# Kernel tuning notes

Hardware: AMD Instinct MI355X
Metric: run time of the kernel (lower is better)

## Reference

```python
import jax, jax.numpy as jnp
import numpy as np

B, NJ, NT, F = 1024, 24, 6, 64
H = 128        # edge/classification MLP hidden width
NODE_OUT = 64  # node MLP output width
REG_OUT = 4


def _mlp2(x, W1, b1, W2, b2):
    h = jax.nn.relu(x @ W1 + b1)
    return jax.nn.relu(h @ W2 + b2)


def _edges(recv, send):
    # broadcast-concat edge formation: (B, Nr, Ns, Fr+Fs)
    Bb, Nr, Fr = recv.shape
    Ns, Fs = send.shape[1], send.shape[2]
    r = jnp.broadcast_to(recv[:, :, None, :], (Bb, Nr, Ns, Fr))
    s = jnp.broadcast_to(send[:, None, :, :], (Bb, Nr, Ns, Fs))
    return jnp.concatenate([r, s], axis=-1)


def _masked_mean(e, mask_send):
    # average-pool edges over sender axis, honoring sender mask
    if mask_send is None:
        return jnp.mean(e, axis=2)
    m = mask_send[:, None, :, :]  # (B,1,Ns,1)
    return jnp.sum(e * m, axis=2) / jnp.maximum(jnp.sum(m, axis=2), 1.0)


def setup_inputs() -> dict:
    key = jax.random.key(0)
    ks = jax.random.split(key, 32)
    g = lambda k, sh, sc: jax.random.normal(k, sh, dtype=jnp.float32) * sc
    inp = {
        "jets": g(ks[0], (B, NJ, F), 1.0),
        "mask": (jax.random.uniform(ks[1], (B, NJ, 1)) < 0.85).astype(jnp.float32),
        "nodes_top": g(ks[2], (B, NT, F), 1.0),
    }
    # edge networks (input = concat of two node feature vectors = 2F)
    for i, name in enumerate(["jj", "jt", "tj"]):
        inp[f"W_{name}1"] = g(ks[3 + 2 * i], (2 * F, H), (2.0 / (2 * F)) ** 0.5)
        inp[f"b_{name}1"] = jnp.zeros((H,), jnp.float32)
        inp[f"W_{name}2"] = g(ks[4 + 2 * i], (H, H), (2.0 / H) ** 0.5)
        inp[f"b_{name}2"] = jnp.zeros((H,), jnp.float32)
    # node networks
    inp["Wnj1"] = g(ks[10], (F + 2 * H, H), (2.0 / (F + 2 * H)) ** 0.5)
    inp["bnj1"] = jnp.zeros((H,), jnp.float32)
    inp["Wnj2"] = g(ks[11], (H, NODE_OUT), (2.0 / H) ** 0.5)
    inp["bnj2"] = jnp.zeros((NODE_OUT,), jnp.float32)
    inp["Wnt1"] = g(ks[12], (F + H, H), (2.0 / (F + H)) ** 0.5)
    inp["bnt1"] = jnp.zeros((H,), jnp.float32)
    inp["Wnt2"] = g(ks[13], (H, NODE_OUT), (2.0 / H) ** 0.5)
    inp["bnt2"] = jnp.zeros((NODE_OUT,), jnp.float32)
    # edge classification network (input = concat of two updated nodes = 2*NODE_OUT)
    inp["Wc1"] = g(ks[14], (2 * NODE_OUT, H), (2.0 / (2 * NODE_OUT)) ** 0.5)
    inp["bc1"] = jnp.zeros((H,), jnp.float32)
    inp["Wc2"] = g(ks[15], (H, H), (2.0 / H) ** 0.5)
    inp["bc2"] = jnp.zeros((H,), jnp.float32)
    inp["Wc3"] = g(ks[16], (H, 1), (2.0 / H) ** 0.5)
    inp["bc3"] = jnp.zeros((1,), jnp.float32)
    inp["Wr1"] = g(ks[17], (NT, NODE_OUT, H), (2.0 / NODE_OUT) ** 0.5)
    inp["br1"] = jnp.zeros((NT, H), jnp.float32)
    inp["Wr2"] = g(ks[18], (NT, H, H), (2.0 / H) ** 0.5)
    inp["br2"] = jnp.zeros((NT, H), jnp.float32)
    inp["Wr3"] = g(ks[19], (NT, H, REG_OUT), (2.0 / H) ** 0.5)
    inp["br3"] = jnp.zeros((NT, REG_OUT), jnp.float32)
    return inp


def reference(jets, mask, nodes_top,
              W_jj1, b_jj1, W_jj2, b_jj2,
              W_jt1, b_jt1, W_jt2, b_jt2,
              W_tj1, b_tj1, W_tj2, b_tj2,
              Wnj1, bnj1, Wnj2, bnj2,
              Wnt1, bnt1, Wnt2, bnt2,
              Wc1, bc1, Wc2, bc2, Wc3, bc3,
              Wr1, br1, Wr2, br2, Wr3, br3):
    # --- TopoGraphLayer ---
    # jet-jet edges (fully connected), masked avg pool over sender jets
    e_jj = _mlp2(_edges(jets, jets), W_jj1, b_jj1, W_jj2, b_jj2)   # (B,NJ,NJ,H)
    pooled_jj = _masked_mean(e_jj, mask)                           # (B,NJ,H)
    # jet-top edges (all top nodes exist -> plain mean pool)
    e_jt = _mlp2(_edges(jets, nodes_top), W_jt1, b_jt1, W_jt2, b_jt2)  # (B,NJ,NT,H)
    pooled_jt = _masked_mean(e_jt, None)                           # (B,NJ,H)
    upd_jets = _mlp2(jnp.concatenate([jets, pooled_jj, pooled_jt], -1),
                     Wnj1, bnj1, Wnj2, bnj2) * mask                # pass_with_mask
    # top-jet edges, masked avg pool over sender jets
    e_tj = _mlp2(_edges(nodes_top, jets), W_tj1, b_tj1, W_tj2, b_tj2)  # (B,NT,NJ,H)
    pooled_tj = _masked_mean(e_tj, mask)                           # (B,NT,H)
    upd_tops = _mlp2(jnp.concatenate([nodes_top, pooled_tj], -1),
                     Wnt1, bnt1, Wnt2, bnt2)                       # (B,NT,NODE_OUT)
    # --- EdgeClassification (top <- jet edges on updated nodes) ---
    e_cls = _mlp2(_edges(upd_tops, upd_jets), Wc1, bc1, Wc2, bc2)  # (B,NT,NJ,H)
    edge_scores = jax.nn.sigmoid(e_cls @ Wc3 + bc3) * mask[:, None, :, :]  # (B,NT,NJ,1)
    # --- ParticlePredictionMLPs (one MLP per top node) ---
    h = jax.nn.relu(jnp.einsum('bpf,pfh->bph', upd_tops, Wr1) + br1)
    h = jax.nn.relu(jnp.einsum('bpf,pfh->bph', h, Wr2) + br2)
    regression = jnp.einsum('bpf,pfh->bph', h, Wr3) + br3          # (B,NT,REG_OUT)
    return upd_jets, upd_tops, edge_scores, regression
```

## Files before the change

### kernel.cpp

```cpp
#include <hip/hip_runtime.h>
#include <hip/hip_bf16.h>


#define DEVI __device__ __forceinline__

typedef __attribute__((ext_vector_type(4))) float  floatx4;
typedef __attribute__((ext_vector_type(8))) __bf16 bf16x8;
typedef __attribute__((ext_vector_type(4))) __bf16 bf16x4;

DEVI float4 f4z() { return make_float4(0.f, 0.f, 0.f, 0.f); }
DEVI float4 f4fma(float a, const float4 b, float4 c) {
    c.x = fmaf(a, b.x, c.x); c.y = fmaf(a, b.y, c.y);
    c.z = fmaf(a, b.z, c.z); c.w = fmaf(a, b.w, c.w);
    return c;
}
DEVI float4 f4add(float4 a, const float4 b) {
    a.x += b.x; a.y += b.y; a.z += b.z; a.w += b.w; return a;
}
DEVI float4 f4relu(float4 a) {
    a.x = fmaxf(a.x, 0.f); a.y = fmaxf(a.y, 0.f);
    a.z = fmaxf(a.z, 0.f); a.w = fmaxf(a.w, 0.f);
    return a;
}
DEVI floatx4 mfma_bf16(bf16x8 a, bf16x8 b, floatx4 c) {
    return __builtin_amdgcn_mfma_f32_16x16x32_bf16(a, b, c, 0, 0, 0);
}

struct PrepJob { const float* src; __bf16* dh; __bf16* dl; int K; int N; };
struct PrepJobs { PrepJob j[4]; };

__global__ __launch_bounds__(256) void prep_kernel(PrepJobs jobs) {
    const PrepJob jb = jobs.j[blockIdx.y];
    const int n = jb.K * jb.N;
    for (int i = blockIdx.x * 256 + threadIdx.x; i < n; i += gridDim.x * 256) {
        const int c = i / jb.K, k = i - c * jb.K;
        const float w = jb.src[(size_t)k * jb.N + c];
        const __bf16 h = (__bf16)w;
        jb.dh[i] = h;
        jb.dl[i] = (__bf16)(w - (float)h);
    }
}

struct PreCfg { const float* X; const float* W; const float* bias; float* out; int nrows; };
struct PreCfg6 { PreCfg c[6]; };

__global__ __launch_bounds__(256) void pre_gemm_kernel(PreCfg6 cfgs) {
    const PreCfg cfg = cfgs.c[blockIdx.y];
    if ((int)blockIdx.x * 32 >= cfg.nrows) return;
    __shared__ float Xs[32][64];
    __shared__ float Ws[64][128];
    const int tid = threadIdx.x;
    {
        const float4* s = (const float4*)(cfg.X + (size_t)blockIdx.x * 2048);
        float4* d = (float4*)&Xs[0][0];
        d[tid] = s[tid]; d[tid + 256] = s[tid + 256];
    }
    {
        const float4* s = (const float4*)cfg.W;
        float4* d = (float4*)&Ws[0][0];
        #pragma unroll
        for (int u = 0; u < 8; ++u) d[tid + u * 256] = s[tid + u * 256];
    }
    __syncthreads();
    const int cg = tid & 31, rg = tid >> 5;
    const int c0 = cg * 4, r0 = rg * 4;
    float4 acc[4] = {f4z(), f4z(), f4z(), f4z()};
    #pragma unroll 4
    for (int k = 0; k < 64; k += 4) {
        const float4 w0 = *(const float4*)&Ws[k + 0][c0];
        const float4 w1 = *(const float4*)&Ws[k + 1][c0];
        const float4 w2 = *(const float4*)&Ws[k + 2][c0];
        const float4 w3 = *(const float4*)&Ws[k + 3][c0];
        #pragma unroll
        for (int i = 0; i < 4; ++i) {
            const float4 x = *(const float4*)&Xs[r0 + i][k];
            acc[i] = f4fma(x.x, w0, acc[i]);
            acc[i] = f4fma(x.y, w1, acc[i]);
            acc[i] = f4fma(x.z, w2, acc[i]);
            acc[i] = f4fma(x.w, w3, acc[i]);
        }
    }
    const float4 bv = cfg.bias ? *(const float4*)(cfg.bias + c0) : f4z();
    #pragma unroll
    for (int i = 0; i < 4; ++i)
        *(float4*)&cfg.out[((size_t)blockIdx.x * 32 + r0 + i) * 128 + c0] = f4add(acc[i], bv);
}

template<int NR, int NS, int EPI, bool MASKED>
__global__ __launch_bounds__(512) void edge_mfma_kernel(
    const float* __restrict__ A, const float* __restrict__ Bp,
    const float* __restrict__ W2, const float* __restrict__ b2,
    const float* __restrict__ mask,
    const float* __restrict__ Wc3, const float* __restrict__ bc3,
    float* __restrict__ out)
{
    constexpr int NE    = NR * NS;
    constexpr int NG    = NE / 48;
    constexpr int RPG   = 48 / NS;
    constexpr int PITCH = 136;
    constexpr int OP    = 132;
    constexpr int POUT_SZ = (EPI == 0) ? 4 : 48 * OP;
    constexpr int PART_SZ = (EPI == 2) ? 48 * 9 : 4;

    __shared__ __bf16 HVh[48 * PITCH];
    __shared__ __bf16 HVl[48 * PITCH];
    __shared__ float  msh[32];
    __shared__ float  POUT[POUT_SZ];
    __shared__ float  part[PART_SZ];

    const int b    = blockIdx.x;
    const int tid  = threadIdx.x;
    const int lane = tid & 63;
    const int wave = tid >> 6;
    const int lhi  = lane >> 4;
    const int llo  = lane & 15;
    const int c    = wave * 16 + llo;

    if (tid < 32) msh[tid] = (tid < NS) ? (MASKED ? mask[b * 24 + tid] : 1.f) : 0.f;

    bf16x8 bh[4], bl[4];
    {
        const float* w2c = W2 + c;
        #pragma unroll
        for (int kc = 0; kc < 4; ++kc) {
            #pragma unroll
            for (int j = 0; j < 8; ++j) {
                const float w = w2c[(size_t)(kc * 32 + lhi * 8 + j) * 128];
                const __bf16 h = (__bf16)w;
                bh[kc][j] = h;
                bl[kc][j] = (__bf16)(w - (float)h);
            }
        }
    }
    const float b2c = b2[c];
    __syncthreads();

    float inv = 1.f;
    if constexpr (EPI != 2) {
        if constexpr (MASKED) {
            float sm = 0.f;
            #pragma unroll
            for (int s = 0; s < NS; ++s) sm += msh[s];
            inv = 1.f / fmaxf(sm, 1.f);
        } else {
            inv = 1.f / (float)NS;
        }
    }

    for (int g = 0; g < NG; ++g) {
        #pragma unroll
        for (int it = 0; it < 3; ++it) {
            const int u = tid + it * 512;
            const int e = u >> 5, kq = u & 31;
            const int r = g * RPG + e / NS;
            const int s = e % NS;
            const float4 a4 = *(const float4*)(A  + ((size_t)b * NR + r) * 128 + kq * 4);
            const float4 p4 = *(const float4*)(Bp + ((size_t)b * NS + s) * 128 + kq * 4);
            const float v[4] = {fmaxf(a4.x + p4.x, 0.f), fmaxf(a4.y + p4.y, 0.f),
                                fmaxf(a4.z + p4.z, 0.f), fmaxf(a4.w + p4.w, 0.f)};
            bf16x4 hh, hl;
            #pragma unroll
            for (int q = 0; q < 4; ++q) {
                const __bf16 h = (__bf16)v[q];
                hh[q] = h;
                hl[q] = (__bf16)(v[q] - (float)h);
            }
            *(bf16x4*)&HVh[e * PITCH + kq * 4] = hh;
            *(bf16x4*)&HVl[e * PITCH + kq * 4] = hl;
        }
        __syncthreads();

        floatx4 accs[3];
        #pragma unroll
        for (int mt = 0; mt < 3; ++mt) {
            const int row = mt * 16 + llo;
            bf16x8 ah[4], al[4];
            #pragma unroll
            for (int kc = 0; kc < 4; ++kc) {
                ah[kc] = *(const bf16x8*)&HVh[row * PITCH + kc * 32 + lhi * 8];
                al[kc] = *(const bf16x8*)&HVl[row * PITCH + kc * 32 + lhi * 8];
            }
            floatx4 acc = {0.f, 0.f, 0.f, 0.f};
            #pragma unroll
            for (int kc = 0; kc < 4; ++kc) {
                acc = mfma_bf16(ah[kc], bh[kc], acc);
                acc = mfma_bf16(al[kc], bh[kc], acc);
                acc = mfma_bf16(ah[kc], bl[kc], acc);
            }
            accs[mt] = acc;
        }

        if constexpr (EPI == 0) {
            float p0 = 0.f, p1 = 0.f;
            #pragma unroll
            for (int mt = 0; mt < 3; ++mt) {
                #pragma unroll
                for (int j = 0; j < 4; ++j) {
                    const int el = mt * 16 + lhi * 4 + j;
                    const int s  = (el >= NS) ? el - NS : el;
                    const float v = fmaxf(accs[mt][j] + b2c, 0.f) * msh[s];
                    if (el >= NS) p1 += v; else p0 += v;
                }
            }
            p0 += __shfl_xor(p0, 16); p0 += __shfl_xor(p0, 32);
            p1 += __shfl_xor(p1, 16); p1 += __shfl_xor(p1, 32);
            if (lhi == 0) {
                out[((size_t)b * NR + g * 2 + 0) * 128 + c] = p0 * inv;
                out[((size_t)b * NR + g * 2 + 1) * 128 + c] = p1 * inv;
            }
            __syncthreads();
        } else if constexpr (EPI == 1) {
            #pragma unroll
            for (int mt = 0; mt < 3; ++mt) {
                #pragma unroll
                for (int j = 0; j < 4; ++j) {
                    const int el = mt * 16 + lhi * 4 + j;
                    const int s  = el % NS;
                    POUT[el * OP + c] = fmaxf(accs[mt][j] + b2c, 0.f) * msh[s];
                }
            }
            __syncthreads();
            for (int u = tid; u < RPG * 128; u += 512) {
                const int rl = u >> 7, cc = u & 127;
                float sm2 = 0.f;
                #pragma unroll
                for (int ss = 0; ss < NS; ++ss) sm2 += POUT[(rl * NS + ss) * OP + cc];
                out[((size_t)b * NR + g * RPG + rl) * 128 + cc] = sm2 * inv;
            }
            __syncthreads();
        } else {
            #pragma unroll
            for (int mt = 0; mt < 3; ++mt) {
                #pragma unroll
                for (int j = 0; j < 4; ++j) {
                    const int el = mt * 16 + lhi * 4 + j;
                    POUT[el * OP + c] = fmaxf(accs[mt][j] + b2c, 0.f);
                }
            }
            __syncthreads();
            if (tid < 384) {
                const int e = tid >> 3, cq = tid & 7;
                float sp = 0.f;
                #pragma unroll
                for (int i = 0; i < 16; ++i)
                    sp += POUT[e * OP + cq * 16 + i] * Wc3[cq * 16 + i];
                part[e * 9 + cq] = sp;
            }
            __syncthreads();
            if (tid < 48) {
                float sm2 = 0.f;
                #pragma unroll
                for (int q = 0; q < 8; ++q) sm2 += part[tid * 9 + q];
                const int rr = g * 2 + (tid >= 24 ? 1 : 0);
                const int ss = (tid >= 24) ? tid - 24 : tid;
                out[((size_t)b * NR + rr) * NS + ss] =
                    msh[ss] / (1.f + expf(-(sm2 + bc3[0])));
            }
            __syncthreads();
        }
    }
}

struct NChunk { const float* base; int stride; };
struct NodeCfg {
    NChunk ch[5]; int nch;
    const __bf16* W1h; const __bf16* W1l; int w1k;
    const float* b1;
    const __bf16* W2h; const __bf16* W2l;
    const float* b2;
    const float* mask;
    float* out;
    int nblk;
};

__global__ __launch_bounds__(512) void node_mfma_kernel(NodeCfg c0, NodeCfg c1) {
    constexpr int XP = 72;
    constexpr int HP = 144;
    __shared__ char smem[2 * 64 * HP * 2];
    __bf16* Xh  = (__bf16*)smem;
    __bf16* Xl  = Xh + 64 * XP;
    __bf16* H1h = (__bf16*)smem;
    __bf16* H1l = H1h + 64 * HP;

    const bool first = (int)blockIdx.x < c0.nblk;
    const NodeCfg& cfg = first ? c0 : c1;
    const int rb  = first ? blockIdx.x : blockIdx.x - c0.nblk;
    const int row0 = rb * 64;

    const int tid  = threadIdx.x;
    const int lane = tid & 63;
    const int wave = tid >> 6;
    const int lhi  = lane >> 4;
    const int llo  = lane & 15;
    const int c    = wave * 16 + llo;

    floatx4 acc[4] = {{0,0,0,0},{0,0,0,0},{0,0,0,0},{0,0,0,0}};
    for (int ch = 0; ch < cfg.nch; ++ch) {
        const NChunk cc = cfg.ch[ch];
        #pragma unroll
        for (int it = 0; it < 2; ++it) {
            const int u = tid + it * 512;
            const int r = u >> 4, kq = u & 15;
            const float4 x4 = *(const float4*)(cc.base + (size_t)(row0 + r) * cc.stride + kq * 4);
            const float v[4] = {x4.x, x4.y, x4.z, x4.w};
            bf16x4 hh, hl;
            #pragma unroll
            for (int q = 0; q < 4; ++q) {
                const __bf16 h = (__bf16)v[q];
                hh[q] = h;
                hl[q] = (__bf16)(v[q] - (float)h);
            }
            *(bf16x4*)&Xh[r * XP + kq * 4] = hh;
            *(bf16x4*)&Xl[r * XP + kq * 4] = hl;
        }
        __syncthreads();
        #pragma unroll
        for (int ks = 0; ks < 2; ++ks) {
            const int kg = ch * 64 + ks * 32 + lhi * 8;
            const bf16x8 bh = *(const bf16x8*)&cfg.W1h[(size_t)c * cfg.w1k + kg];
            const bf16x8 bl = *(const bf16x8*)&cfg.W1l[(size_t)c * cfg.w1k + kg];
            #pragma unroll
            for (int mt = 0; mt < 4; ++mt) {
                const int ro = (mt * 16 + llo) * XP + ks * 32 + lhi * 8;
                const bf16x8 ah = *(const bf16x8*)&Xh[ro];
                const bf16x8 al = *(const bf16x8*)&Xl[ro];
                acc[mt] = mfma_bf16(ah, bh, acc[mt]);
                acc[mt] = mfma_bf16(al, bh, acc[mt]);
                acc[mt] = mfma_bf16(ah, bl, acc[mt]);
            }
        }
        __syncthreads();
    }

    {
        const float b1c = cfg.b1[c];
        #pragma unroll
        for (int mt = 0; mt < 4; ++mt) {
            #pragma unroll
            for (int j = 0; j < 4; ++j) {
                const int row = mt * 16 + lhi * 4 + j;
                const float v = fmaxf(acc[mt][j] + b1c, 0.f);
                const __bf16 h = (__bf16)v;
                const int blk = (c >> 3) ^ (row & 7);
                const int off = row * HP + blk * 8 + (c & 7);
                H1h[off] = h;
                H1l[off] = (__bf16)(v - (float)h);
            }
        }
    }
    __syncthreads();

    const int ct2 = wave & 3;
    const int c2  = ct2 * 16 + llo;
    const int mtb = wave >> 2;
    floatx4 acc2[2] = {{0,0,0,0},{0,0,0,0}};
    #pragma unroll
    for (int ks = 0; ks < 4; ++ks) {
        const int kg = ks * 32 + lhi * 8;
        const bf16x8 bh = *(const bf16x8*)&cfg.W2h[(size_t)c2 * 128 + kg];
        const bf16x8 bl = *(const bf16x8*)&cfg.W2l[(size_t)c2 * 128 + kg];
        #pragma unroll
        for (int i = 0; i < 2; ++i) {
            const int row = (mtb + i * 2) * 16 + llo;
            const int blk = (ks * 4 + lhi) ^ (row & 7);
            const bf16x8 ah = *(const bf16x8*)&H1h[row * HP + blk * 8];
            const bf16x8 al = *(const bf16x8*)&H1l[row * HP + blk * 8];
            acc2[i] = mfma_bf16(ah, bh, acc2[i]);
            acc2[i] = mfma_bf16(al, bh, acc2[i]);
            acc2[i] = mfma_bf16(ah, bl, acc2[i]);
        }
    }
    {
        const float b2c = cfg.b2[c2];
        #pragma unroll
        for (int i = 0; i < 2; ++i) {
            #pragma unroll
            for (int j = 0; j < 4; ++j) {
                const int row = (mtb + i * 2) * 16 + lhi * 4 + j;
                float v = fmaxf(acc2[i][j] + b2c, 0.f);
                if (cfg.mask) v *= cfg.mask[row0 + row];
                cfg.out[(size_t)(row0 + row) * 64 + c2] = v;
            }
        }
    }
}

__global__ __launch_bounds__(256) void reg_kernel(
    const float* __restrict__ tops_upd,
    const float* __restrict__ Wr1, const float* __restrict__ br1,
    const float* __restrict__ Wr2, const float* __restrict__ br2,
    const float* __restrict__ Wr3, const float* __restrict__ br3,
    float* __restrict__ outp) {
    const int t = blockIdx.y, bc = blockIdx.x, tid = threadIdx.x;
    __shared__ float Xs[32][64];
    __shared__ float h1[32][128];
    __shared__ float h2[32][132];
    __shared__ float W3s[512];
    for (int u = tid; u < 512; u += 256) {
        const int r = u >> 4, k4 = (u & 15) * 4;
        *(float4*)&Xs[r][k4] =
            *(const float4*)(tops_upd + ((size_t)(bc * 32 + r) * 6 + t) * 64 + k4);
    }
    for (int u = tid; u < 512; u += 256) W3s[u] = Wr3[t * 512 + u];
    __syncthreads();

    const int cg = tid & 31, rg = tid >> 5;
    const int c0 = cg * 4, r0 = rg * 4;
    const float* W1 = Wr1 + (size_t)t * 64 * 128;
    float4 acc[4];
    #pragma unroll
    for (int i = 0; i < 4; ++i) acc[i] = f4z();
    #pragma unroll 4
    for (int k = 0; k < 64; k += 4) {
        const float4 w0 = *(const float4*)(W1 + (size_t)(k + 0) * 128 + c0);
        const float4 w1 = *(const float4*)(W1 + (size_t)(k + 1) * 128 + c0);
        const float4 w2 = *(const float4*)(W1 + (size_t)(k + 2) * 128 + c0);
        const float4 w3 = *(const float4*)(W1 + (size_t)(k + 3) * 128 + c0);
        #pragma unroll
        for (int i = 0; i < 4; ++i) {
            const float4 x = *(const float4*)&Xs[r0 + i][k];
            acc[i] = f4fma(x.x, w0, acc[i]);
            acc[i] = f4fma(x.y, w1, acc[i]);
            acc[i] = f4fma(x.z, w2, acc[i]);
            acc[i] = f4fma(x.w, w3, acc[i]);
        }
    }
    const float4 b1v = *(const float4*)(br1 + t * 128 + c0);
    #pragma unroll
    for (int i = 0; i < 4; ++i)
        *(float4*)&h1[r0 + i][c0] = f4relu(f4add(acc[i], b1v));
    __syncthreads();

    const float* W2 = Wr2 + (size_t)t * 128 * 128;
    #pragma unroll
    for (int i = 0; i < 4; ++i) acc[i] = f4z();
    #pragma unroll 4
    for (int k = 0; k < 128; k += 4) {
        const float4 w0 = *(const float4*)(W2 + (size_t)(k + 0) * 128 + c0);
        const float4 w1 = *(const float4*)(W2 + (size_t)(k + 1) * 128 + c0);
        const float4 w2 = *(const float4*)(W2 + (size_t)(k + 2) * 128 + c0);
        const float4 w3 = *(const float4*)(W2 + (size_t)(k + 3) * 128 + c0);
        #pragma unroll
        for (int i = 0; i < 4; ++i) {
            const float4 h = *(const float4*)&h1[r0 + i][k];
            acc[i] = f4fma(h.x, w0, acc[i]);
            acc[i] = f4fma(h.y, w1, acc[i]);
            acc[i] = f4fma(h.z, w2, acc[i]);
            acc[i] = f4fma(h.w, w3, acc[i]);
        }
    }
    const float4 b2v = *(const float4*)(br2 + t * 128 + c0);
    #pragma unroll
    for (int i = 0; i < 4; ++i)
        *(float4*)&h2[r0 + i][c0] = f4relu(f4add(acc[i], b2v));
    __syncthreads();

    if (tid < 128) {
        const int r = tid >> 2, cc = tid & 3;
        float a = 0.f;
        #pragma unroll 4
        for (int k = 0; k < 128; k += 4) {
            const float4 h = *(const float4*)&h2[r][k];
            a = fmaf(h.x, W3s[(k + 0) * 4 + cc], a);
            a = fmaf(h.y, W3s[(k + 1) * 4 + cc], a);
            a = fmaf(h.z, W3s[(k + 2) * 4 + cc], a);
            a = fmaf(h.w, W3s[(k + 3) * 4 + cc], a);
        }
        outp[((size_t)(bc * 32 + r) * 6 + t) * 4 + cc] = a + br3[t * 4 + cc];
    }
}

extern "C" void kernel_launch(void* const* d_in, const int* in_sizes, int n_in,
                              void* d_out, int out_size, void* d_ws, size_t ws_size,
                              hipStream_t stream) {
    const float* jets  = (const float*)d_in[0];
    const float* mask  = (const float*)d_in[1];
    const float* tops  = (const float*)d_in[2];
    const float* W_jj1 = (const float*)d_in[3];
    const float* b_jj1 = (const float*)d_in[4];
    const float* W_jj2 = (const float*)d_in[5];
    const float* b_jj2 = (const float*)d_in[6];
    const float* W_jt1 = (const float*)d_in[7];
    const float* b_jt1 = (const float*)d_in[8];
    const float* W_jt2 = (const float*)d_in[9];
    const float* b_jt2 = (const float*)d_in[10];
    const float* W_tj1 = (const float*)d_in[11];
    const float* b_tj1 = (const float*)d_in[12];
    const float* W_tj2 = (const float*)d_in[13];
    const float* b_tj2 = (const float*)d_in[14];
    const float* Wnj1  = (const float*)d_in[15];
    const float* bnj1  = (const float*)d_in[16];
    const float* Wnj2  = (const float*)d_in[17];
    const float* bnj2  = (const float*)d_in[18];
    const float* Wnt1  = (const float*)d_in[19];
    const float* bnt1  = (const float*)d_in[20];
    const float* Wnt2  = (const float*)d_in[21];
    const float* bnt2  = (const float*)d_in[22];
    const float* Wc1   = (const float*)d_in[23];
    const float* bc1   = (const float*)d_in[24];
    const float* Wc2   = (const float*)d_in[25];
    const float* bc2   = (const float*)d_in[26];
    const float* Wc3   = (const float*)d_in[27];
    const float* bc3   = (const float*)d_in[28];
    const float* Wr1   = (const float*)d_in[29];
    const float* br1   = (const float*)d_in[30];
    const float* Wr2   = (const float*)d_in[31];
    const float* br2   = (const float*)d_in[32];
    const float* Wr3   = (const float*)d_in[33];
    const float* br3   = (const float*)d_in[34];

    float* ws = (float*)d_ws;
    constexpr size_t SZ_J = (size_t)1024 * 24 * 128;
    constexpr size_t SZ_T = (size_t)1024 * 6 * 128;
    float* Ajj = ws;
    float* Bjj = Ajj + SZ_J;
    float* Ajt = Bjj + SZ_J;
    float* Btj = Ajt + SZ_J;
    float* Atj = Btj + SZ_J;
    float* Bjt = Atj + SZ_T;
    float* Pjj = Bjt + SZ_T;
    float* Pjt = Pjj + SZ_J;
    float* Ptj = Pjt + SZ_J;
    float* Acc = Ptj + SZ_T;
    float* Bcc = Acc + SZ_T;

    __bf16* W1njT_h = (__bf16*)Acc;
    __bf16* W1njT_l = W1njT_h + 320 * 128;
    __bf16* W2njT_h = W1njT_l + 320 * 128;
    __bf16* W2njT_l = W2njT_h + 128 * 64;
    __bf16* W1ntT_h = W2njT_l + 128 * 64;
    __bf16* W1ntT_l = W1ntT_h + 192 * 128;
    __bf16* W2ntT_h = W1ntT_l + 192 * 128;
    __bf16* W2ntT_l = W2ntT_h + 128 * 64;

    float* outp     = (float*)d_out;
    float* upd_jets = outp;
    float* upd_tops = outp + (size_t)1024 * 24 * 64;
    float* scores   = upd_tops + (size_t)1024 * 6 * 64;
    float* regr     = scores + (size_t)1024 * 6 * 24;

    {
        PrepJobs pj;
        pj.j[0] = {Wnj1, W1njT_h, W1njT_l, 320, 128};
        pj.j[1] = {Wnj2, W2njT_h, W2njT_l, 128, 64};
        pj.j[2] = {Wnt1, W1ntT_h, W1ntT_l, 192, 128};
        pj.j[3] = {Wnt2, W2ntT_h, W2ntT_l, 128, 64};
        prep_kernel<<<dim3(160, 4), 256, 0, stream>>>(pj);
    }
    {
        PreCfg6 cfg;
        cfg.c[0] = {jets, W_jj1,            b_jj1,  Ajj, 24576};
        cfg.c[1] = {jets, W_jj1 + 64 * 128, nullptr, Bjj, 24576};
        cfg.c[2] = {jets, W_jt1,            b_jt1,  Ajt, 24576};
        cfg.c[3] = {jets, W_tj1 + 64 * 128, nullptr, Btj, 24576};
        cfg.c[4] = {tops, W_tj1,            b_tj1,  Atj, 6144};
        cfg.c[5] = {tops, W_jt1 + 64 * 128, nullptr, Bjt, 6144};
        pre_gemm_kernel<<<dim3(768, 6), 256, 0, stream>>>(cfg);
    }
    edge_mfma_kernel<24, 24, 0, true ><<<1024, 512, 0, stream>>>(
        Ajj, Bjj, W_jj2, b_jj2, mask, nullptr, nullptr, Pjj);
    edge_mfma_kernel<24,  6, 1, false><<<1024, 512, 0, stream>>>(
        Ajt, Bjt, W_jt2, b_jt2, nullptr, nullptr, nullptr, Pjt);
    edge_mfma_kernel< 6, 24, 0, true ><<<1024, 512, 0, stream>>>(
        Atj, Btj, W_tj2, b_tj2, mask, nullptr, nullptr, Ptj);

    {
        NodeCfg cj, ct;
        cj.ch[0] = {jets, 64};
        cj.ch[1] = {Pjj, 128};      cj.ch[2] = {Pjj + 64, 128};
        cj.ch[3] = {Pjt, 128};      cj.ch[4] = {Pjt + 64, 128};
        cj.nch = 5;
        cj.W1h = W1njT_h; cj.W1l = W1njT_l; cj.w1k = 320; cj.b1 = bnj1;
        cj.W2h = W2njT_h; cj.W2l = W2njT_l; cj.b2 = bnj2;
        cj.mask = mask; cj.out = upd_jets; cj.nblk = 384;

        ct.ch[0] = {tops, 64};
        ct.ch[1] = {Ptj, 128};      ct.ch[2] = {Ptj + 64, 128};
        ct.ch[3] = {nullptr, 0};    ct.ch[4] = {nullptr, 0};
        ct.nch = 3;
        ct.W1h = W1ntT_h; ct.W1l = W1ntT_l; ct.w1k = 192; ct.b1 = bnt1;
        ct.W2h = W2ntT_h; ct.W2l = W2ntT_l; ct.b2 = bnt2;
        ct.mask = nullptr; ct.out = upd_tops; ct.nblk = 96;

        node_mfma_kernel<<<480, 512, 0, stream>>>(cj, ct);
    }

    {
        PreCfg6 cfg;
        cfg.c[0] = {upd_jets, Wc1 + 64 * 128, nullptr, Bcc, 24576};
        cfg.c[1] = {upd_tops, Wc1,            bc1,     Acc, 6144};
        for (int i = 2; i < 6; ++i) cfg.c[i] = {nullptr, nullptr, nullptr, nullptr, 0};
        pre_gemm_kernel<<<dim3(768, 2), 256, 0, stream>>>(cfg);
    }
    edge_mfma_kernel< 6, 24, 2, true ><<<1024, 512, 0, stream>>>(
        Acc, Bcc, Wc2, bc2, mask, Wc3, bc3, scores);
    reg_kernel<<<dim3(32, 6), 256, 0, stream>>>(upd_tops, Wr1, br1, Wr2, br2, Wr3, br3, regr);
}
```

Measured before the change: 325.0 us.

## Double-buffer edge hidden tiles and prefetch next group in jj edge kernel

```diff
diff --git a/kernel.cpp b/kernel.cpp
--- a/kernel.cpp
+++ b/kernel.cpp
@@ -87,7 +87,7 @@
 }
 
 template<int NR, int NS, int EPI, bool MASKED>
-__global__ __launch_bounds__(512) void edge_mfma_kernel(
+__global__ __launch_bounds__(512, (EPI == 0) ? 6 : 4) void edge_mfma_kernel(
     const float* __restrict__ A, const float* __restrict__ Bp,
     const float* __restrict__ W2, const float* __restrict__ b2,
     const float* __restrict__ mask,
@@ -99,11 +99,12 @@
     constexpr int RPG   = 48 / NS;
     constexpr int PITCH = 136;
     constexpr int OP    = 132;
+    constexpr int NBUF  = (EPI == 0) ? 2 : 1;
     constexpr int POUT_SZ = (EPI == 0) ? 4 : 48 * OP;
     constexpr int PART_SZ = (EPI == 2) ? 48 * 9 : 4;
 
-    __shared__ __bf16 HVh[48 * PITCH];
-    __shared__ __bf16 HVl[48 * PITCH];
+    __shared__ __bf16 HVh[NBUF][48 * PITCH];
+    __shared__ __bf16 HVl[NBUF][48 * PITCH];
     __shared__ float  msh[32];
     __shared__ float  POUT[POUT_SZ];
     __shared__ float  part[PART_SZ];
@@ -147,17 +148,25 @@
         }
     }
 
-    for (int g = 0; g < NG; ++g) {
+    float4 ra[3], rp[3];
+    auto load_regs = [&](int g) {
         #pragma unroll
         for (int it = 0; it < 3; ++it) {
             const int u = tid + it * 512;
             const int e = u >> 5, kq = u & 31;
             const int r = g * RPG + e / NS;
             const int s = e % NS;
-            const float4 a4 = *(const float4*)(A  + ((size_t)b * NR + r) * 128 + kq * 4);
-            const float4 p4 = *(const float4*)(Bp + ((size_t)b * NS + s) * 128 + kq * 4);
-            const float v[4] = {fmaxf(a4.x + p4.x, 0.f), fmaxf(a4.y + p4.y, 0.f),
-                                fmaxf(a4.z + p4.z, 0.f), fmaxf(a4.w + p4.w, 0.f)};
+            ra[it] = *(const float4*)(A  + ((size_t)b * NR + r) * 128 + kq * 4);
+            rp[it] = *(const float4*)(Bp + ((size_t)b * NS + s) * 128 + kq * 4);
+        }
+    };
+    auto store_buf = [&](int bi) {
+        #pragma unroll
+        for (int it = 0; it < 3; ++it) {
+            const int u = tid + it * 512;
+            const int e = u >> 5, kq = u & 31;
+            const float v[4] = {fmaxf(ra[it].x + rp[it].x, 0.f), fmaxf(ra[it].y + rp[it].y, 0.f),
+                                fmaxf(ra[it].z + rp[it].z, 0.f), fmaxf(ra[it].w + rp[it].w, 0.f)};
             bf16x4 hh, hl;
             #pragma unroll
             for (int q = 0; q < 4; ++q) {
@@ -165,98 +174,117 @@
                 hh[q] = h;
                 hl[q] = (__bf16)(v[q] - (float)h);
             }
-            *(bf16x4*)&HVh[e * PITCH + kq * 4] = hh;
-            *(bf16x4*)&HVl[e * PITCH + kq * 4] = hl;
-        }
-        __syncthreads();
-
-        floatx4 accs[3];
+            *(bf16x4*)&HVh[bi][e * PITCH + kq * 4] = hh;
+            *(bf16x4*)&HVl[bi][e * PITCH + kq * 4] = hl;
+        }
+    };
+    auto compute = [&](int bi, floatx4* accs) {
         #pragma unroll
         for (int mt = 0; mt < 3; ++mt) {
             const int row = mt * 16 + llo;
-            bf16x8 ah[4], al[4];
+            floatx4 acc = {0.f, 0.f, 0.f, 0.f};
             #pragma unroll
             for (int kc = 0; kc < 4; ++kc) {
-                ah[kc] = *(const bf16x8*)&HVh[row * PITCH + kc * 32 + lhi * 8];
-                al[kc] = *(const bf16x8*)&HVl[row * PITCH + kc * 32 + lhi * 8];
-            }
-            floatx4 acc = {0.f, 0.f, 0.f, 0.f};
-            #pragma unroll
-            for (int kc = 0; kc < 4; ++kc) {
-                acc = mfma_bf16(ah[kc], bh[kc], acc);
-                acc = mfma_bf16(al[kc], bh[kc], acc);
-                acc = mfma_bf16(ah[kc], bl[kc], acc);
+                const bf16x8 ah = *(const bf16x8*)&HVh[bi][row * PITCH + kc * 32 + lhi * 8];
+                const bf16x8 al = *(const bf16x8*)&HVl[bi][row * PITCH + kc * 32 + lhi * 8];
+                acc = mfma_bf16(ah, bh[kc], acc);
+                acc = mfma_bf16(al, bh[kc], acc);
+                acc = mfma_bf16(ah, bl[kc], acc);
             }
             accs[mt] = acc;
         }
-
-        if constexpr (EPI == 0) {
-            float p0 = 0.f, p1 = 0.f;
-            #pragma unroll
-            for (int mt = 0; mt < 3; ++mt) {
+    };
+
+    if constexpr (EPI == 0) {
+        load_regs(0);
+        store_buf(0);
+        __syncthreads();
+        int cur = 0;
+        for (int g = 0; g < NG; ++g) {
+            const bool more = (g + 1 < NG);
+            if (more) load_regs(g + 1);
+            floatx4 accs[3];
+            compute(cur, accs);
+            {
+                float p0 = 0.f, p1 = 0.f;
                 #pragma unroll
-                for (int j = 0; j < 4; ++j) {
-                    const int el = mt * 16 + lhi * 4 + j;
-                    const int s  = (el >= NS) ? el - NS : el;
-                    const float v = fmaxf(accs[mt][j] + b2c, 0.f) * msh[s];
-                    if (el >= NS) p1 += v; else p0 += v;
+                for (int mt = 0; mt < 3; ++mt) {
+                    #pragma unroll
+                    for (int j = 0; j < 4; ++j) {
+                        const int el = mt * 16 + lhi * 4 + j;
+                        const int s  = (el >= NS) ? el - NS : el;
+                        const float v = fmaxf(accs[mt][j] + b2c, 0.f) * msh[s];
+                        if (el >= NS) p1 += v; else p0 += v;
+                    }
                 }
-            }
-            p0 += __shfl_xor(p0, 16); p0 += __shfl_xor(p0, 32);
-            p1 += __shfl_xor(p1, 16); p1 += __shfl_xor(p1, 32);
-            if (lhi == 0) {
-                out[((size_t)b * NR + g * 2 + 0) * 128 + c] = p0 * inv;
-                out[((size_t)b * NR + g * 2 + 1) * 128 + c] = p1 * inv;
-            }
+                p0 += __shfl_xor(p0, 16); p0 += __shfl_xor(p0, 32);
+                p1 += __shfl_xor(p1, 16); p1 += __shfl_xor(p1, 32);
+                if (lhi == 0) {
+                    out[((size_t)b * NR + g * 2 + 0) * 128 + c] = p0 * inv;
+                    out[((size_t)b * NR + g * 2 + 1) * 128 + c] = p1 * inv;
+                }
+            }
+            if (more) store_buf(cur ^ 1);
             __syncthreads();
-        } else if constexpr (EPI == 1) {
-            #pragma unroll
-            for (int mt = 0; mt < 3; ++mt) {
+            cur ^= 1;
+        }
+    } else {
+        for (int g = 0; g < NG; ++g) {
+            load_regs(g);
+            store_buf(0);
+            __syncthreads();
+            floatx4 accs[3];
+            compute(0, accs);
+
+            if constexpr (EPI == 1) {
                 #pragma unroll
-                for (int j = 0; j < 4; ++j) {
-                    const int el = mt * 16 + lhi * 4 + j;
-                    const int s  = el % NS;
-                    POUT[el * OP + c] = fmaxf(accs[mt][j] + b2c, 0.f) * msh[s];
+                for (int mt = 0; mt < 3; ++mt) {
+                    #pragma unroll
+                    for (int j = 0; j < 4; ++j) {
+                        const int el = mt * 16 + lhi * 4 + j;
+                        const int s  = el % NS;
+                        POUT[el * OP + c] = fmaxf(accs[mt][j] + b2c, 0.f) * msh[s];
+                    }
                 }
-            }
-            __syncthreads();
-            for (int u = tid; u < RPG * 128; u += 512) {
-                const int rl = u >> 7, cc = u & 127;
-                float sm2 = 0.f;
+                __syncthreads();
+                for (int u = tid; u < RPG * 128; u += 512) {
+                    const int rl = u >> 7, cc = u & 127;
+                    float sm2 = 0.f;
+                    #pragma unroll
+                    for (int ss = 0; ss < NS; ++ss) sm2 += POUT[(rl * NS + ss) * OP + cc];
+                    out[((size_t)b * NR + g * RPG + rl) * 128 + cc] = sm2 * inv;
+                }
+                __syncthreads();
+            } else {
                 #pragma unroll
-                for (int ss = 0; ss < NS; ++ss) sm2 += POUT[(rl * NS + ss) * OP + cc];
-                out[((size_t)b * NR + g * RPG + rl) * 128 + cc] = sm2 * inv;
-            }
-            __syncthreads();
-        } else {
-            #pragma unroll
-            for (int mt = 0; mt < 3; ++mt) {
-                #pragma unroll
-                for (int j = 0; j < 4; ++j) {
-                    const int el = mt * 16 + lhi * 4 + j;
-                    POUT[el * OP + c] = fmaxf(accs[mt][j] + b2c, 0.f);
+                for (int mt = 0; mt < 3; ++mt) {
+                    #pragma unroll
+                    for (int j = 0; j < 4; ++j) {
+                        const int el = mt * 16 + lhi * 4 + j;
+                        POUT[el * OP + c] = fmaxf(accs[mt][j] + b2c, 0.f);
+                    }
                 }
-            }
-            __syncthreads();
-            if (tid < 384) {
-                const int e = tid >> 3, cq = tid & 7;
-                float sp = 0.f;
-                #pragma unroll
-                for (int i = 0; i < 16; ++i)
-                    sp += POUT[e * OP + cq * 16 + i] * Wc3[cq * 16 + i];
-                part[e * 9 + cq] = sp;
-            }
-            __syncthreads();
-            if (tid < 48) {
-                float sm2 = 0.f;
-                #pragma unroll
-                for (int q = 0; q < 8; ++q) sm2 += part[tid * 9 + q];
-                const int rr = g * 2 + (tid >= 24 ? 1 : 0);
-                const int ss = (tid >= 24) ? tid - 24 : tid;
-                out[((size_t)b * NR + rr) * NS + ss] =
-                    msh[ss] / (1.f + expf(-(sm2 + bc3[0])));
-            }
-            __syncthreads();
+                __syncthreads();
+                if (tid < 384) {
+                    const int e = tid >> 3, cq = tid & 7;
+                    float sp = 0.f;
+                    #pragma unroll
+                    for (int i = 0; i < 16; ++i)
+                        sp += POUT[e * OP + cq * 16 + i] * Wc3[cq * 16 + i];
+                    part[e * 9 + cq] = sp;
+                }
+                __syncthreads();
+                if (tid < 48) {
+                    float sm2 = 0.f;
+                    #pragma unroll
+                    for (int q = 0; q < 8; ++q) sm2 += part[tid * 9 + q];
+                    const int rr = g * 2 + (tid >= 24 ? 1 : 0);
+                    const int ss = (tid >= 24) ? tid - 24 : tid;
+                    out[((size_t)b * NR + rr) * NS + ss] =
+                        msh[ss] / (1.f + expf(-(sm2 + bc3[0])));
+                }
+                __syncthreads();
+            }
         }
     }
 }
```

After: 395.9 us. +21.8%, slower.
